# Kernel tuning notes

Measured on AMD Instinct MI355X. Metric: run time of the kernel, lower is better.

## Reference

```python
import jax, jax.numpy as jnp
import numpy as np

D_MODEL = 160
D_STATE = 64
D_CONV = 12
N_BLOCKS = 8
CONV_K = 9
D_INNER = 2 * D_MODEL          # expand=2 -> 320
DT_RANK = (D_MODEL + 15) // 16  # ceil(160/16) = 10
B, T = 16, 2048


def setup_inputs() -> dict:
    key = jax.random.key(0)
    ks = jax.random.split(key, 10)
    rn = lambda k, shape, s=0.02: jax.random.normal(k, shape, dtype=jnp.float32) * s
    x = jax.random.normal(ks[0], (B, T, 1), dtype=jnp.float32)
    pre_w = rn(ks[1], (D_MODEL, 1, CONV_K), 0.3)
    pre_b = jnp.zeros((D_MODEL,), jnp.float32)
    ln_g = jnp.ones((N_BLOCKS, D_MODEL), jnp.float32)
    ln_b = jnp.zeros((N_BLOCKS, D_MODEL), jnp.float32)
    in_w = rn(ks[2], (N_BLOCKS, 2 * D_INNER, D_MODEL))
    conv_w = rn(ks[3], (N_BLOCKS, D_INNER, D_CONV), 0.1)
    conv_b = jnp.zeros((N_BLOCKS, D_INNER), jnp.float32)
    xproj_w = rn(ks[4], (N_BLOCKS, DT_RANK + 2 * D_STATE, D_INNER))
    dt_w = rn(ks[5], (N_BLOCKS, D_INNER, DT_RANK), 0.1)
    # softplus-inverse of dt_init=0.01 (mamba-style init) so softplus(dt_b) ~ 0.01
    dt_b = jnp.full((N_BLOCKS, D_INNER), float(np.log(np.expm1(0.01))), jnp.float32)
    A_log = jnp.log(jnp.tile(jnp.arange(1, D_STATE + 1, dtype=jnp.float32)[None, None, :],
                             (N_BLOCKS, D_INNER, 1)))
    D_skip = jnp.ones((N_BLOCKS, D_INNER), jnp.float32)
    out_w = rn(ks[6], (N_BLOCKS, D_MODEL, D_INNER))
    head_w = rn(ks[7], (1, D_MODEL))
    head_b = jnp.zeros((1,), jnp.float32)
    return dict(x=x, pre_w=pre_w, pre_b=pre_b, ln_g=ln_g, ln_b=ln_b, in_w=in_w,
                conv_w=conv_w, conv_b=conv_b, xproj_w=xproj_w, dt_w=dt_w, dt_b=dt_b,
                A_log=A_log, D_skip=D_skip, out_w=out_w, head_w=head_w, head_b=head_b)


def _layernorm(x, g, b, eps=1e-5):
    m = jnp.mean(x, -1, keepdims=True)
    v = jnp.var(x, -1, keepdims=True)
    return (x - m) * jax.lax.rsqrt(v + eps) * g + b


def _mamba(x, in_w, conv_w, conv_b, xproj_w, dt_w, dt_b, A_log, D_skip, out_w):
    # x: (B, L, d_model)
    bsz, L, _ = x.shape
    xz = jnp.einsum('bld,ed->ble', x, in_w)          # (B, L, 2*D_INNER)
    u, z = jnp.split(xz, 2, axis=-1)
    # depthwise causal conv over time
    u_c = jnp.moveaxis(u, 1, 2)                       # (B, D_INNER, L)
    u_c = jax.lax.conv_general_dilated(
        u_c, conv_w[:, None, :], (1,), [(D_CONV - 1, 0)],
        dimension_numbers=('NCH', 'OIH', 'NCH'), feature_group_count=D_INNER)
    u = jax.nn.silu(jnp.moveaxis(u_c, 1, 2) + conv_b)  # (B, L, D_INNER)
    x_dbl = jnp.einsum('bld,ed->ble', u, xproj_w)      # (B, L, DT_RANK + 2*D_STATE)
    dt, Bm, Cm = jnp.split(x_dbl, [DT_RANK, DT_RANK + D_STATE], axis=-1)
    delta = jax.nn.softplus(jnp.einsum('blr,dr->bld', dt, dt_w) + dt_b)  # (B, L, D_INNER)
    A = -jnp.exp(A_log)                                # (D_INNER, D_STATE)

    def step(h, ins):
        d_t, B_t, C_t, u_t = ins                       # (B,di),(B,ds),(B,ds),(B,di)
        dA = jnp.exp(d_t[:, :, None] * A)              # (B, di, ds)
        h = h * dA + (d_t * u_t)[:, :, None] * B_t[:, None, :]
        y = jnp.einsum('bds,bs->bd', h, C_t)
        return h, y

    tm = lambda a: jnp.moveaxis(a, 1, 0)               # time-major
    h0 = jnp.zeros((bsz, D_INNER, D_STATE), x.dtype)
    _, ys = jax.lax.scan(step, h0, (tm(delta), tm(Bm), tm(Cm), tm(u)))
    y = jnp.moveaxis(ys, 0, 1) + u * D_skip            # (B, L, D_INNER)
    y = y * jax.nn.silu(z)
    return jnp.einsum('bld,ed->ble', y, out_w)         # (B, L, d_model)


def reference(x, pre_w, pre_b, ln_g, ln_b, in_w, conv_w, conv_b, xproj_w,
              dt_w, dt_b, A_log, D_skip, out_w, head_w, head_b):
    # conv stem: (B,T,1) -> (B,1,T) -> conv -> (B,d_model,T)
    h = jax.lax.conv_general_dilated(
        jnp.moveaxis(x, 1, 2), pre_w, (1,), [(CONV_K // 2, CONV_K // 2)],
        dimension_numbers=('NCH', 'OIH', 'NCH')) + pre_b[None, :, None]
    h = jax.nn.gelu(jnp.moveaxis(h, 1, 2), approximate=False)  # torch GELU exact
    for i in range(N_BLOCKS):
        res = h
        y = _layernorm(h, ln_g[i], ln_b[i])
        y = _mamba(y, in_w[i], conv_w[i], conv_b[i], xproj_w[i], dt_w[i],
                   dt_b[i], A_log[i], D_skip[i], out_w[i])
        h = y + res  # dropout is identity at inference
    out = jnp.einsum('bld,od->blo', h, head_w) + head_b
    return out[..., 0]                                 # (B, T)
```

## Files before the change

### kernel.cpp

```cpp
#include <hip/hip_runtime.h>
#include <math.h>

#define BATCH 16
#define TLEN 2048
#define NTOK (BATCH*TLEN)
#define DMODEL 160
#define DINNER 320
#define DSTATE 64
#define DTRANK 10
#define XDBL 138
#define XP 140
#define DCONV 12
#define PREK 9
#define NBLK 8

typedef __attribute__((ext_vector_type(8))) short short8;
typedef __attribute__((ext_vector_type(4))) float floatx4;

__device__ __forceinline__ float sigmoidf_(float x) { return 1.f / (1.f + __expf(-x)); }
__device__ __forceinline__ unsigned short f2bf(float f) {
  union { float f; unsigned u; } v; v.f = f;
  unsigned r = v.u + 0x7FFF + ((v.u >> 16) & 1);
  return (unsigned short)(r >> 16);
}
__device__ __forceinline__ float bf2f(unsigned short s) {
  union { unsigned u; float f; } v; v.u = ((unsigned)s) << 16;
  return v.f;
}
__device__ __forceinline__ float bflo(unsigned u) {
  union { unsigned u; float f; } v; v.u = u << 16; return v.f;
}
__device__ __forceinline__ float bfhi(unsigned u) {
  union { unsigned u; float f; } v; v.u = u & 0xFFFF0000u; return v.f;
}

__global__ __launch_bounds__(256)
void k_preconv(const float* __restrict__ x, const float* __restrict__ w,
               const float* __restrict__ bias, float* __restrict__ h) {
  int gid = blockIdx.x * 256 + threadIdx.x;
  if (gid >= NTOK * DMODEL) return;
  int c = gid % DMODEL;
  int tok = gid / DMODEL;
  int b = tok / TLEN, t = tok % TLEN;
  const float* xb = x + (size_t)b * TLEN;
  float acc = bias[c];
#pragma unroll
  for (int k = 0; k < PREK; ++k) {
    int tp = t + k - PREK / 2;
    float xv = (tp >= 0 && tp < TLEN) ? xb[tp] : 0.f;
    acc = fmaf(w[c * PREK + k], xv, acc);
  }
  h[gid] = 0.5f * acc * (1.f + erff(acc * 0.70710678118654752440f));
}

__global__ __launch_bounds__(256)
void k_cast(const float* __restrict__ iw, const float* __restrict__ xw,
            const float* __restrict__ ow, unsigned short* __restrict__ wbf) {
  int i = blockIdx.x * 256 + threadIdx.x;
  if (i < 102400) wbf[i] = f2bf(iw[i]);
  else if (i < 146560) wbf[i] = f2bf(xw[i - 102400]);
  else if (i < 197760) wbf[i] = f2bf(ow[i - 146560]);
}

__global__ __launch_bounds__(256)
void k_ln(const float* __restrict__ h, const float* __restrict__ g,
          const float* __restrict__ bb, unsigned short* __restrict__ y) {
  int row = blockIdx.x * 4 + (threadIdx.x >> 6);
  int lane = threadIdx.x & 63;
  const float* hr = h + (size_t)row * DMODEL;
  float v0 = hr[lane], v1 = hr[lane + 64];
  float v2 = (lane < DMODEL - 128) ? hr[lane + 128] : 0.f;
  float s = v0 + v1 + v2;
  float sq = v0 * v0 + v1 * v1 + v2 * v2;
#pragma unroll
  for (int off = 32; off; off >>= 1) {
    s += __shfl_xor(s, off);
    sq += __shfl_xor(sq, off);
  }
  float mean = s * (1.f / DMODEL);
  float var = sq * (1.f / DMODEL) - mean * mean;
  float rstd = rsqrtf(var + 1e-5f);
  unsigned short* yr = y + (size_t)row * DMODEL;
  yr[lane] = f2bf((v0 - mean) * rstd * g[lane] + bb[lane]);
  yr[lane + 64] = f2bf((v1 - mean) * rstd * g[lane + 64] + bb[lane + 64]);
  if (lane < DMODEL - 128)
    yr[lane + 128] = f2bf((v2 - mean) * rstd * g[lane + 128] + bb[lane + 128]);
}

__global__ __launch_bounds__(256)
void k_mm_in(const unsigned short* __restrict__ A, const unsigned short* __restrict__ Wb,
             float* __restrict__ xout, unsigned short* __restrict__ zout) {
  __shared__ short As[128 * 40];
  __shared__ short Ws[128 * 40];
  int tid = threadIdx.x;
  int m0 = blockIdx.y * 128, n0 = blockIdx.x * 128;
  int w = tid >> 6, lane = tid & 63;
  int rm = (w >> 1) * 64, cn = (w & 1) * 64;
  int lm = lane & 15, quad = lane >> 4;
  int r = tid >> 1, seg = tid & 1;
  const unsigned short* pA = A + (size_t)(m0 + r) * DMODEL + seg * 16;
  const unsigned short* pW = Wb + (size_t)(n0 + r) * DMODEL + seg * 16;
  floatx4 acc[4][4];
#pragma unroll
  for (int i = 0; i < 4; ++i)
#pragma unroll
    for (int j = 0; j < 4; ++j)
      acc[i][j] = (floatx4){0.f, 0.f, 0.f, 0.f};
  for (int kt = 0; kt < 5; ++kt) {
    uint4 a0 = *(const uint4*)(pA + kt * 32);
    uint4 a1 = *(const uint4*)(pA + kt * 32 + 8);
    uint4 w0 = *(const uint4*)(pW + kt * 32);
    uint4 w1 = *(const uint4*)(pW + kt * 32 + 8);
    *(short8*)&As[r * 40 + seg * 16]     = *(short8*)&a0;
    *(short8*)&As[r * 40 + seg * 16 + 8] = *(short8*)&a1;
    *(short8*)&Ws[r * 40 + seg * 16]     = *(short8*)&w0;
    *(short8*)&Ws[r * 40 + seg * 16 + 8] = *(short8*)&w1;
    __syncthreads();
    short8 af[4], wf[4];
#pragma unroll
    for (int i = 0; i < 4; ++i)
      af[i] = *(short8*)&As[(rm + i * 16 + lm) * 40 + quad * 8];
#pragma unroll
    for (int j = 0; j < 4; ++j)
      wf[j] = *(short8*)&Ws[(cn + j * 16 + lm) * 40 + quad * 8];
#pragma unroll
    for (int i = 0; i < 4; ++i)
#pragma unroll
      for (int j = 0; j < 4; ++j)
        acc[i][j] = __builtin_amdgcn_mfma_f32_16x16x32_bf16(af[i], wf[j], acc[i][j], 0, 0, 0);
    __syncthreads();
  }
#pragma unroll
  for (int i = 0; i < 4; ++i)
#pragma unroll
    for (int reg = 0; reg < 4; ++reg) {
      int m = m0 + rm + i * 16 + quad * 4 + reg;
#pragma unroll
      for (int j = 0; j < 4; ++j) {
        int n = n0 + cn + j * 16 + lm;
        float v = acc[i][j][reg];
        if (n < DINNER) xout[(size_t)m * DINNER + n] = v;
        else zout[(size_t)m * DINNER + n - DINNER] = f2bf(v);
      }
    }
}

__global__ __launch_bounds__(256)
void k_mm_g(const unsigned short* __restrict__ A, const unsigned short* __restrict__ Wb,
            float* __restrict__ C, const float* __restrict__ resid, int N, int K) {
  __shared__ short As[128 * 40];
  __shared__ short Ws[64 * 40];
  int tid = threadIdx.x;
  int m0 = blockIdx.y * 128, n0 = blockIdx.x * 64;
  int w = tid >> 6, lane = tid & 63;
  int rm = w * 32;
  int lm = lane & 15, quad = lane >> 4;
  int r = tid >> 1, seg = tid & 1;
  int wr = tid >> 2, wseg = tid & 3;
  bool wvld = (n0 + wr) < N;
  const unsigned short* pA = A + (size_t)(m0 + r) * K + seg * 16;
  const unsigned short* pW = Wb + (size_t)(wvld ? (n0 + wr) : 0) * K + wseg * 8;
  floatx4 acc[2][4];
#pragma unroll
  for (int i = 0; i < 2; ++i)
#pragma unroll
    for (int j = 0; j < 4; ++j)
      acc[i][j] = (floatx4){0.f, 0.f, 0.f, 0.f};
  int nk = K >> 5;
  for (int kt = 0; kt < nk; ++kt) {
    uint4 a0 = *(const uint4*)(pA + kt * 32);
    uint4 a1 = *(const uint4*)(pA + kt * 32 + 8);
    uint4 wv = wvld ? *(const uint4*)(pW + kt * 32)
                    : make_uint4(0u, 0u, 0u, 0u);
    *(short8*)&As[r * 40 + seg * 16]     = *(short8*)&a0;
    *(short8*)&As[r * 40 + seg * 16 + 8] = *(short8*)&a1;
    *(short8*)&Ws[wr * 40 + wseg * 8]    = *(short8*)&wv;
    __syncthreads();
    short8 af[2], wf[4];
#pragma unroll
    for (int i = 0; i < 2; ++i)
      af[i] = *(short8*)&As[(rm + i * 16 + lm) * 40 + quad * 8];
#pragma unroll
    for (int j = 0; j < 4; ++j)
      wf[j] = *(short8*)&Ws[(j * 16 + lm) * 40 + quad * 8];
#pragma unroll
    for (int i = 0; i < 2; ++i)
#pragma unroll
      for (int j = 0; j < 4; ++j)
        acc[i][j] = __builtin_amdgcn_mfma_f32_16x16x32_bf16(af[i], wf[j], acc[i][j], 0, 0, 0);
    __syncthreads();
  }
#pragma unroll
  for (int i = 0; i < 2; ++i)
#pragma unroll
    for (int reg = 0; reg < 4; ++reg) {
      int m = m0 + rm + i * 16 + quad * 4 + reg;
#pragma unroll
      for (int j = 0; j < 4; ++j) {
        int n = n0 + j * 16 + lm;
        if (n < N) {
          float v = acc[i][j][reg];
          if (resid) v += resid[(size_t)m * N + n];
          C[(size_t)m * N + n] = v;
        }
      }
    }
}

__global__ __launch_bounds__(256)
void k_mm_x(const unsigned short* __restrict__ A, const unsigned short* __restrict__ Wb,
            unsigned short* __restrict__ C) {
  const int N = XDBL, K = DINNER;
  __shared__ short As[128 * 40];
  __shared__ short Ws[64 * 40];
  int tid = threadIdx.x;
  int m0 = blockIdx.y * 128, n0 = blockIdx.x * 64;
  int w = tid >> 6, lane = tid & 63;
  int rm = w * 32;
  int lm = lane & 15, quad = lane >> 4;
  int r = tid >> 1, seg = tid & 1;
  int wr = tid >> 2, wseg = tid & 3;
  bool wvld = (n0 + wr) < N;
  const unsigned short* pA = A + (size_t)(m0 + r) * K + seg * 16;
  const unsigned short* pW = Wb + (size_t)(wvld ? (n0 + wr) : 0) * K + wseg * 8;
  floatx4 acc[2][4];
#pragma unroll
  for (int i = 0; i < 2; ++i)
#pragma unroll
    for (int j = 0; j < 4; ++j)
      acc[i][j] = (floatx4){0.f, 0.f, 0.f, 0.f};
  int nk = K >> 5;
  for (int kt = 0; kt < nk; ++kt) {
    uint4 a0 = *(const uint4*)(pA + kt * 32);
    uint4 a1 = *(const uint4*)(pA + kt * 32 + 8);
    uint4 wv = wvld ? *(const uint4*)(pW + kt * 32)
                    : make_uint4(0u, 0u, 0u, 0u);
    *(short8*)&As[r * 40 + seg * 16]     = *(short8*)&a0;
    *(short8*)&As[r * 40 + seg * 16 + 8] = *(short8*)&a1;
    *(short8*)&Ws[wr * 40 + wseg * 8]    = *(short8*)&wv;
    __syncthreads();
    short8 af[2], wf[4];
#pragma unroll
    for (int i = 0; i < 2; ++i)
      af[i] = *(short8*)&As[(rm + i * 16 + lm) * 40 + quad * 8];
#pragma unroll
    for (int j = 0; j < 4; ++j)
      wf[j] = *(short8*)&Ws[(j * 16 + lm) * 40 + quad * 8];
#pragma unroll
    for (int i = 0; i < 2; ++i)
#pragma unroll
      for (int j = 0; j < 4; ++j)
        acc[i][j] = __builtin_amdgcn_mfma_f32_16x16x32_bf16(af[i], wf[j], acc[i][j], 0, 0, 0);
    __syncthreads();
  }
#pragma unroll
  for (int i = 0; i < 2; ++i)
#pragma unroll
    for (int reg = 0; reg < 4; ++reg) {
      int m = m0 + rm + i * 16 + quad * 4 + reg;
#pragma unroll
      for (int j = 0; j < 4; ++j) {
        int n = n0 + j * 16 + lm;
        if (n < N) {
          int slot = (n < DTRANK) ? n
                   : (n < DTRANK + DSTATE) ? 12 + 2 * (n - DTRANK)
                                           : 13 + 2 * (n - DTRANK - DSTATE);
          C[(size_t)m * XP + slot] = f2bf(acc[i][j][reg]);
        }
      }
    }
}

__global__ __launch_bounds__(256)
void k_convT(const float* __restrict__ xbuf, const float* __restrict__ cw,
             const float* __restrict__ cb, unsigned short* __restrict__ uTb,
             unsigned short* __restrict__ ubf) {
  int t0 = blockIdx.x * 64, d0 = blockIdx.y * 64, b = blockIdx.z;
  __shared__ float xs[76 * 65];
  __shared__ float us[64 * 65];
  int tid = threadIdx.x, j = tid & 63, w = tid >> 6;
#pragma unroll
  for (int it = 0; it < 19; ++it) {
    int r = it * 4 + w;
    int t = t0 - (DCONV - 1) + r;
    xs[r * 65 + j] = (t >= 0 && t < TLEN)
        ? xbuf[((size_t)b * TLEN + t) * DINNER + d0 + j] : 0.f;
  }
  __syncthreads();
  float cwr[DCONV];
#pragma unroll
  for (int k = 0; k < DCONV; ++k) cwr[k] = cw[(d0 + j) * DCONV + k];
  float cbv = cb[d0 + j];
#pragma unroll
  for (int it = 0; it < 16; ++it) {
    int tl = it * 4 + w;
    float acc = cbv;
#pragma unroll
    for (int k = 0; k < DCONV; ++k)
      acc = fmaf(cwr[k], xs[(tl + k) * 65 + j], acc);
    us[tl * 65 + j] = acc * sigmoidf_(acc);
  }
  __syncthreads();
#pragma unroll
  for (int it = 0; it < 16; ++it) {
    int tr = it * 4 + w;
    ubf[((size_t)b * TLEN + t0 + tr) * DINNER + d0 + j] = f2bf(us[tr * 65 + j]);
  }
#pragma unroll
  for (int it = 0; it < 16; ++it) {
    int dl = it * 4 + w;
    uTb[((size_t)b * DINNER + d0 + dl) * TLEN + t0 + j] = f2bf(us[j * 65 + dl]);
  }
}

__global__ __launch_bounds__(256)
void k_pack(const unsigned short* __restrict__ zbuf, const unsigned short* __restrict__ xdbl,
            const unsigned short* __restrict__ uTb,
            const float* __restrict__ dtw, const float* __restrict__ dtb,
            const float* __restrict__ Dskip,
            float2* __restrict__ qT, unsigned* __restrict__ eT) {
  int t0 = blockIdx.x * 64, d0 = blockIdx.y * 64, b = blockIdx.z;
  __shared__ float zs[64 * 65];
  __shared__ float xd[64 * 13];
  int tid = threadIdx.x, j = tid & 63, w = tid >> 6;
#pragma unroll
  for (int it = 0; it < 16; ++it) {
    int i = it * 4 + w;
    zs[i * 65 + j] = bf2f(zbuf[((size_t)b * TLEN + t0 + i) * DINNER + d0 + j]);
  }
  {
    int r = tid >> 2, c = tid & 3;
    size_t rowb = ((size_t)b * TLEN + t0 + r) * XP;
    for (int cc = c; cc < DTRANK; cc += 4)
      xd[r * 13 + cc] = bf2f(xdbl[rowb + cc]);
  }
  __syncthreads();
#pragma unroll
  for (int it = 0; it < 16; ++it) {
    int dl = it * 4 + w, d = d0 + dl;
    float acc = dtb[d];
    const float* wr = dtw + d * DTRANK;
#pragma unroll
    for (int rr = 0; rr < DTRANK; ++rr)
      acc = fmaf(xd[j * 13 + rr], wr[rr], acc);
    float del = (acc > 20.f) ? acc : log1pf(__expf(acc));
    size_t o = ((size_t)b * DINNER + d) * TLEN + t0 + j;
    float uv = bf2f(uTb[o]);
    float zv = zs[j * 65 + dl];
    float ssz = zv * sigmoidf_(zv);
    qT[o] = make_float2(del, del * uv);
    unsigned lo = f2bf(uv * Dskip[d] * ssz);
    unsigned hi = f2bf(ssz);
    eT[o] = lo | (hi << 16);
  }
}

__global__ __launch_bounds__(256)
void k_scan(const float2* __restrict__ qT, const unsigned* __restrict__ eT,
            const unsigned short* __restrict__ xdbl, const float* __restrict__ Alog,
            unsigned short* __restrict__ yTb) {
  int wave = threadIdx.x >> 6, lane = threadIdx.x & 63;
  int b = blockIdx.x / (DINNER / 4);
  int d = (blockIdx.x % (DINNER / 4)) * 4 + wave;
  __shared__ float ps_all[4][16 * 68];
  float* ps = ps_all[wave];
  float Al2 = -__expf(Alog[d * DSTATE + lane]) * 1.44269504088896340736f;
  size_t chan = ((size_t)b * DINNER + d) * TLEN;
  const float2* pq = qT + chan;
  const unsigned* pe = eT + chan;
  unsigned short* py = yTb + chan;
  const unsigned* xb = (const unsigned*)(xdbl + (size_t)b * TLEN * XP) + 6 + lane;
  float h = 0.f;
  int tl = lane & 15, qq = lane >> 4;
  for (int t0 = 0; t0 < TLEN; t0 += 16) {
#pragma unroll
    for (int t = 0; t < 16; ++t) {
      float2 q = pq[t0 + t];
      unsigned bc = xb[(size_t)(t0 + t) * (XP / 2)];
      float Bv = bflo(bc), Cv = bfhi(bc);
      h = fmaf(h, exp2f(q.x * Al2), q.y * Bv);
      ps[t * 68 + lane] = h * Cv;
    }
    float p = 0.f;
    const floatx4* pr = (const floatx4*)&ps[tl * 68 + qq * 16];
#pragma unroll
    for (int i = 0; i < 4; ++i) {
      floatx4 v = pr[i];
      p += v[0] + v[1] + v[2] + v[3];
    }
    p += __shfl_xor(p, 16);
    p += __shfl_xor(p, 32);
    if (lane < 16) {
      int t = t0 + tl;
      unsigned e = pe[t];
      py[t] = f2bf(fmaf(p, bfhi(e), bflo(e)));
    }
  }
}

__global__ __launch_bounds__(256)
void k_t2b(const unsigned short* __restrict__ yTb, unsigned short* __restrict__ ybf) {
  int t0 = blockIdx.x * 64, d0 = blockIdx.y * 64, b = blockIdx.z;
  __shared__ unsigned short ls[64 * 66];
  int tid = threadIdx.x, j = tid & 63, w = tid >> 6;
#pragma unroll
  for (int it = 0; it < 16; ++it) {
    int dl = it * 4 + w;
    ls[dl * 66 + j] = yTb[((size_t)b * DINNER + d0 + dl) * TLEN + t0 + j];
  }
  __syncthreads();
#pragma unroll
  for (int it = 0; it < 16; ++it) {
    int tr = it * 4 + w;
    ybf[((size_t)b * TLEN + t0 + tr) * DINNER + d0 + j] = ls[j * 66 + tr];
  }
}

__global__ __launch_bounds__(256)
void k_head(const float* __restrict__ h, const float* __restrict__ hw,
            const float* __restrict__ hb, float* __restrict__ out) {
  int tok = blockIdx.x * 4 + (threadIdx.x >> 6);
  int lane = threadIdx.x & 63;
  const float* hr = h + (size_t)tok * DMODEL;
  float s = hr[lane] * hw[lane] + hr[lane + 64] * hw[lane + 64];
  if (lane < DMODEL - 128) s += hr[lane + 128] * hw[lane + 128];
#pragma unroll
  for (int off = 32; off; off >>= 1) s += __shfl_xor(s, off);
  if (lane == 0) out[tok] = s + hb[0];
}

extern "C" void kernel_launch(void* const* d_in, const int* in_sizes, int n_in,
                              void* d_out, int out_size, void* d_ws, size_t ws_size,
                              hipStream_t stream) {
  const float* x      = (const float*)d_in[0];
  const float* pre_w  = (const float*)d_in[1];
  const float* pre_b  = (const float*)d_in[2];
  const float* ln_g   = (const float*)d_in[3];
  const float* ln_b   = (const float*)d_in[4];
  const float* in_w   = (const float*)d_in[5];
  const float* conv_w = (const float*)d_in[6];
  const float* conv_b = (const float*)d_in[7];
  const float* xproj_w= (const float*)d_in[8];
  const float* dt_w   = (const float*)d_in[9];
  const float* dt_b   = (const float*)d_in[10];
  const float* A_log  = (const float*)d_in[11];
  const float* D_skip = (const float*)d_in[12];
  const float* out_w  = (const float*)d_in[13];
  const float* head_w = (const float*)d_in[14];
  const float* head_b = (const float*)d_in[15];
  float* out = (float*)d_out;

  float* ws = (float*)d_ws;
  float* h    = ws;
  unsigned short* xdbl_bf = (unsigned short*)(h + (size_t)NTOK * DMODEL);
  float2* qT  = (float2*)(xdbl_bf + (size_t)NTOK * XP);
  unsigned short* uT_bf = (unsigned short*)(qT + (size_t)NTOK * DINNER);
  float* X    = (float*)(uT_bf + (size_t)NTOK * DINNER);
  float* Y    = X + (size_t)NTOK * DINNER;
  unsigned short* wbf = (unsigned short*)(Y + (size_t)NTOK * DINNER / 2);

  unsigned short* lnxd_bf = (unsigned short*)qT;
  unsigned short* u_bf    = (unsigned short*)qT;
  float*          xbuf    = X;
  unsigned*       eT      = (unsigned*)X;
  unsigned short* y_bf    = (unsigned short*)X;
  unsigned short* zbuf_bf = (unsigned short*)Y;
  unsigned short* yT_bf   = (unsigned short*)Y;
  unsigned short* w_in    = wbf;
  unsigned short* w_xp    = wbf + 102400;
  unsigned short* w_ou    = wbf + 146560;

  k_preconv<<<NTOK * DMODEL / 256, 256, 0, stream>>>(x, pre_w, pre_b, h);

  for (int L = 0; L < NBLK; ++L) {
    k_cast<<<773, 256, 0, stream>>>(
        in_w + (size_t)L * 640 * DMODEL, xproj_w + (size_t)L * XDBL * DINNER,
        out_w + (size_t)L * DMODEL * DINNER, wbf);
    k_ln<<<NTOK / 4, 256, 0, stream>>>(h, ln_g + L * DMODEL, ln_b + L * DMODEL, lnxd_bf);
    k_mm_in<<<dim3(5, NTOK / 128), 256, 0, stream>>>(lnxd_bf, w_in, xbuf, zbuf_bf);
    k_convT<<<dim3(TLEN / 64, DINNER / 64, BATCH), 256, 0, stream>>>(
        xbuf, conv_w + (size_t)L * DINNER * DCONV, conv_b + (size_t)L * DINNER,
        uT_bf, u_bf);
    k_mm_x<<<dim3(3, NTOK / 128), 256, 0, stream>>>(u_bf, w_xp, xdbl_bf);
    k_pack<<<dim3(TLEN / 64, DINNER / 64, BATCH), 256, 0, stream>>>(
        zbuf_bf, xdbl_bf, uT_bf, dt_w + (size_t)L * DINNER * DTRANK,
        dt_b + (size_t)L * DINNER, D_skip + (size_t)L * DINNER, qT, eT);
    k_scan<<<BATCH * (DINNER / 4), 256, 0, stream>>>(
        qT, eT, xdbl_bf, A_log + (size_t)L * DINNER * DSTATE, yT_bf);
    k_t2b<<<dim3(TLEN / 64, DINNER / 64, BATCH), 256, 0, stream>>>(yT_bf, y_bf);
    k_mm_g<<<dim3(3, NTOK / 128), 256, 0, stream>>>(y_bf, w_ou, h, h, DMODEL, DINNER);
  }

  k_head<<<NTOK / 4, 256, 0, stream>>>(h, head_w, head_b, out);
}
```

Baseline: 3.640 ms.

## Scan two channels per wave and batch all weight casts into one launch

```diff
diff --git a/kernel.cpp b/kernel.cpp
--- a/kernel.cpp
+++ b/kernel.cpp
@@ -13,6 +13,7 @@
 #define DCONV 12
 #define PREK 9
 #define NBLK 8
+#define WPL 197760
 
 typedef __attribute__((ext_vector_type(8))) short short8;
 typedef __attribute__((ext_vector_type(4))) float floatx4;
@@ -56,10 +57,12 @@
 __global__ __launch_bounds__(256)
 void k_cast(const float* __restrict__ iw, const float* __restrict__ xw,
             const float* __restrict__ ow, unsigned short* __restrict__ wbf) {
-  int i = blockIdx.x * 256 + threadIdx.x;
-  if (i < 102400) wbf[i] = f2bf(iw[i]);
-  else if (i < 146560) wbf[i] = f2bf(xw[i - 102400]);
-  else if (i < 197760) wbf[i] = f2bf(ow[i - 146560]);
+  int L = blockIdx.x / 773;
+  int i = (blockIdx.x % 773) * 256 + threadIdx.x;
+  unsigned short* wl = wbf + (size_t)L * WPL;
+  if (i < 102400) wl[i] = f2bf(iw[(size_t)L * 102400 + i]);
+  else if (i < 146560) wl[i] = f2bf(xw[(size_t)L * 44160 + i - 102400]);
+  else if (i < WPL) wl[i] = f2bf(ow[(size_t)L * 51200 + i - 146560]);
 }
 
 __global__ __launch_bounds__(256)
@@ -355,45 +358,55 @@
   }
 }
 
-__global__ __launch_bounds__(256)
+__global__ __launch_bounds__(128)
 void k_scan(const float2* __restrict__ qT, const unsigned* __restrict__ eT,
             const unsigned short* __restrict__ xdbl, const float* __restrict__ Alog,
             unsigned short* __restrict__ yTb) {
   int wave = threadIdx.x >> 6, lane = threadIdx.x & 63;
-  int b = blockIdx.x / (DINNER / 4);
-  int d = (blockIdx.x % (DINNER / 4)) * 4 + wave;
-  __shared__ float ps_all[4][16 * 68];
-  float* ps = ps_all[wave];
-  float Al2 = -__expf(Alog[d * DSTATE + lane]) * 1.44269504088896340736f;
-  size_t chan = ((size_t)b * DINNER + d) * TLEN;
-  const float2* pq = qT + chan;
-  const unsigned* pe = eT + chan;
-  unsigned short* py = yTb + chan;
+  int b = blockIdx.x / 80;
+  int d0 = (blockIdx.x % 80) * 4 + wave * 2;
+  __shared__ float2 ps_all[2][16 * 66];
+  float2* psw = ps_all[wave];
+  float Al2a = -__expf(Alog[d0 * DSTATE + lane]) * 1.44269504088896340736f;
+  float Al2b = -__expf(Alog[(d0 + 1) * DSTATE + lane]) * 1.44269504088896340736f;
+  size_t chan0 = ((size_t)b * DINNER + d0) * TLEN;
+  const float2* pq0 = qT + chan0;
+  const float2* pq1 = pq0 + TLEN;
+  const unsigned* pe0 = eT + chan0;
+  const unsigned* pe1 = pe0 + TLEN;
+  unsigned short* py0 = yTb + chan0;
+  unsigned short* py1 = py0 + TLEN;
   const unsigned* xb = (const unsigned*)(xdbl + (size_t)b * TLEN * XP) + 6 + lane;
-  float h = 0.f;
+  float2 h2 = make_float2(0.f, 0.f);
   int tl = lane & 15, qq = lane >> 4;
   for (int t0 = 0; t0 < TLEN; t0 += 16) {
 #pragma unroll
     for (int t = 0; t < 16; ++t) {
-      float2 q = pq[t0 + t];
+      float2 q0 = pq0[t0 + t];
+      float2 q1 = pq1[t0 + t];
       unsigned bc = xb[(size_t)(t0 + t) * (XP / 2)];
       float Bv = bflo(bc), Cv = bfhi(bc);
-      h = fmaf(h, exp2f(q.x * Al2), q.y * Bv);
-      ps[t * 68 + lane] = h * Cv;
+      float ea = exp2f(q0.x * Al2a);
+      float eb = exp2f(q1.x * Al2b);
+      h2.x = fmaf(h2.x, ea, q0.y * Bv);
+      h2.y = fmaf(h2.y, eb, q1.y * Bv);
+      psw[t * 66 + lane] = make_float2(h2.x * Cv, h2.y * Cv);
     }
-    float p = 0.f;
-    const floatx4* pr = (const floatx4*)&ps[tl * 68 + qq * 16];
-#pragma unroll
-    for (int i = 0; i < 4; ++i) {
+    float px = 0.f, py = 0.f;
+    const floatx4* pr = (const floatx4*)&psw[tl * 66 + qq * 16];
+#pragma unroll
+    for (int i = 0; i < 8; ++i) {
       floatx4 v = pr[i];
-      p += v[0] + v[1] + v[2] + v[3];
+      px += v[0] + v[2];
+      py += v[1] + v[3];
     }
-    p += __shfl_xor(p, 16);
-    p += __shfl_xor(p, 32);
+    px += __shfl_xor(px, 16); py += __shfl_xor(py, 16);
+    px += __shfl_xor(px, 32); py += __shfl_xor(py, 32);
     if (lane < 16) {
       int t = t0 + tl;
-      unsigned e = pe[t];
-      py[t] = f2bf(fmaf(p, bfhi(e), bflo(e)));
+      unsigned e0 = pe0[t], e1 = pe1[t];
+      py0[t] = f2bf(fmaf(px, bfhi(e0), bflo(e0)));
+      py1[t] = f2bf(fmaf(py, bfhi(e1), bflo(e1)));
     }
   }
 }
@@ -466,16 +479,14 @@
   unsigned short* y_bf    = (unsigned short*)X;
   unsigned short* zbuf_bf = (unsigned short*)Y;
   unsigned short* yT_bf   = (unsigned short*)Y;
-  unsigned short* w_in    = wbf;
-  unsigned short* w_xp    = wbf + 102400;
-  unsigned short* w_ou    = wbf + 146560;
 
   k_preconv<<<NTOK * DMODEL / 256, 256, 0, stream>>>(x, pre_w, pre_b, h);
+  k_cast<<<NBLK * 773, 256, 0, stream>>>(in_w, xproj_w, out_w, wbf);
 
   for (int L = 0; L < NBLK; ++L) {
-    k_cast<<<773, 256, 0, stream>>>(
-        in_w + (size_t)L * 640 * DMODEL, xproj_w + (size_t)L * XDBL * DINNER,
-        out_w + (size_t)L * DMODEL * DINNER, wbf);
+    unsigned short* w_in = wbf + (size_t)L * WPL;
+    unsigned short* w_xp = w_in + 102400;
+    unsigned short* w_ou = w_in + 146560;
     k_ln<<<NTOK / 4, 256, 0, stream>>>(h, ln_g + L * DMODEL, ln_b + L * DMODEL, lnxd_bf);
     k_mm_in<<<dim3(5, NTOK / 128), 256, 0, stream>>>(lnxd_bf, w_in, xbuf, zbuf_bf);
     k_convT<<<dim3(TLEN / 64, DINNER / 64, BATCH), 256, 0, stream>>>(
@@ -485,7 +496,7 @@
     k_pack<<<dim3(TLEN / 64, DINNER / 64, BATCH), 256, 0, stream>>>(
         zbuf_bf, xdbl_bf, uT_bf, dt_w + (size_t)L * DINNER * DTRANK,
         dt_b + (size_t)L * DINNER, D_skip + (size_t)L * DINNER, qT, eT);
-    k_scan<<<BATCH * (DINNER / 4), 256, 0, stream>>>(
+    k_scan<<<BATCH * 80, 128, 0, stream>>>(
         qT, eT, xdbl_bf, A_log + (size_t)L * DINNER * DSTATE, yT_bf);
     k_t2b<<<dim3(TLEN / 64, DINNER / 64, BATCH), 256, 0, stream>>>(yT_bf, y_bf);
     k_mm_g<<<dim3(3, NTOK / 128), 256, 0, stream>>>(y_bf, w_ou, h, h, DMODEL, DINNER);
```

After: 4.011 ms. 1.1x slower.
